# Kernel tuning notes

Measured on AMD Instinct MI355X. Metric: run time of the kernel, lower is better.

## Reference

```python
import jax, jax.numpy as jnp
import numpy as np

S, T = 8192, 16          # words per sentence, max chars per word
EC, HC = 64, 128         # char embed dim, char LSTM hidden
DW, HW = 300, 256        # word embed dim, word LSTM hidden
VW, VC, TAGS = 50000, 128, 50
DIN = DW + 2 * HC        # word LSTM input dim


def _lstm_scan(x, Wih, Whh, b, reverse=False):
    """Single-direction LSTM over x: [T, N, E] -> outputs [T, N, H].
    PyTorch gate order (i, f, g, o); b = b_ih + b_hh combined."""
    N = x.shape[1]
    H = Whh.shape[1]
    h0 = jnp.zeros((N, H), x.dtype)

    def cell(carry, xt):
        h, c = carry
        g = xt @ Wih.T + h @ Whh.T + b
        i, f, gg, o = jnp.split(g, 4, axis=-1)
        c = jax.nn.sigmoid(f) * c + jax.nn.sigmoid(i) * jnp.tanh(gg)
        h = jax.nn.sigmoid(o) * jnp.tanh(c)
        return (h, c), h

    _, hs = jax.lax.scan(cell, (h0, h0), x, reverse=reverse)
    return hs


def setup_inputs() -> dict:
    key = jax.random.key(0)
    ks = iter(jax.random.split(key, 40))
    p = lambda *shape: jax.random.normal(next(ks), shape, jnp.float32) * 0.05

    inp = {
        "word_ix": jax.random.randint(next(ks), (S,), 0, VW, jnp.int32),
        "char_ix": jax.random.randint(next(ks), (S, T), 0, VC, jnp.int32),
        "char_len": jax.random.randint(next(ks), (S,), 1, T + 1, jnp.int32),
        "word_emb": p(VW, DW),
        "char_emb": p(VC, EC),
        # char LSTM, 2 layers x 2 directions (dir axis leading)
        "cW_ih0": p(2, 4 * HC, EC), "cW_hh0": p(2, 4 * HC, HC), "cb0": p(2, 4 * HC),
        "cW_ih1": p(2, 4 * HC, 2 * HC), "cW_hh1": p(2, 4 * HC, HC), "cb1": p(2, 4 * HC),
        # word LSTM, 2 layers x 2 directions
        "wW_ih0": p(2, 4 * HW, DIN), "wW_hh0": p(2, 4 * HW, HW), "wb0": p(2, 4 * HW),
        "wW_ih1": p(2, 4 * HW, 2 * HW), "wW_hh1": p(2, 4 * HW, HW), "wb1": p(2, 4 * HW),
        "out_W": p(TAGS, 2 * HW), "out_b": p(TAGS),
    }
    return inp


def reference(word_ix, char_ix, char_len, word_emb, char_emb,
              cW_ih0, cW_hh0, cb0, cW_ih1, cW_hh1, cb1,
              wW_ih0, wW_hh0, wb0, wW_ih1, wW_hh1, wb1,
              out_W, out_b):
    # --- char LSTM: all words batched together ---
    x = char_emb[char_ix].transpose(1, 0, 2)  # [T, S, EC]
    # NOTE: original calls the bidirectional LSTM one char at a time while
    # carrying hidden state, so the "backward" direction also scans forward.
    h0f = _lstm_scan(x, cW_ih0[0], cW_hh0[0], cb0[0])
    h0b = _lstm_scan(x, cW_ih0[1], cW_hh0[1], cb0[1])
    o0 = jnp.concatenate([h0f, h0b], -1)       # [T, S, 2*HC]
    h1f = _lstm_scan(o0, cW_ih1[0], cW_hh1[0], cb1[0])
    h1b = _lstm_scan(o0, cW_ih1[1], cW_hh1[1], cb1[1])
    o1 = jnp.concatenate([h1f, h1b], -1)       # [T, S, 2*HC]
    # last valid char per word (ragged lengths)
    chars_repr = o1[char_len - 1, jnp.arange(S)]  # [S, 2*HC]

    # --- word LSTM: true biLSTM over the sentence, batch 1 ---
    wx = jnp.concatenate([word_emb[word_ix], chars_repr], -1)[:, None, :]  # [S,1,DIN]
    w0f = _lstm_scan(wx, wW_ih0[0], wW_hh0[0], wb0[0])
    w0b = _lstm_scan(wx, wW_ih0[1], wW_hh0[1], wb0[1], reverse=True)
    wo0 = jnp.concatenate([w0f, w0b], -1)      # [S, 1, 2*HW]
    w1f = _lstm_scan(wo0, wW_ih1[0], wW_hh1[0], wb1[0])
    w1b = _lstm_scan(wo0, wW_ih1[1], wW_hh1[1], wb1[1], reverse=True)
    wo1 = jnp.concatenate([w1f, w1b], -1).reshape(S, 2 * HW)

    logits = wo1 @ out_W.T + out_b             # [S, TAGS]
    return jax.nn.log_softmax(logits, axis=1)
```

## Files before the change

### kernel.cpp

```cpp
#include <hip/hip_runtime.h>
#include <math.h>


#define SW 8192
#define TC 16
#define ECD 64
#define HCD 128
#define DWD 300
#define HWD 256
#define DIND 556
#define NTAGS 50
#define SENT 0x40000000u

typedef float f32x4 __attribute__((ext_vector_type(4)));

__device__ __forceinline__ float sigf(float x) { return 1.f / (1.f + expf(-x)); }

#define BM 64
#define BN 64
#define BK 16

__global__ __launch_bounds__(256) void gemm2(
    const float* __restrict__ A1, int lda1, const int* __restrict__ idx1,
    const float* __restrict__ W1, int ldw1, int K1,
    const float* __restrict__ A2, int lda2,
    const float* __restrict__ W2, int ldw2, int K2,
    const float* __restrict__ bias, float* __restrict__ C, int N, int ldc)
{
    __shared__ float As[BK][BM + 4];
    __shared__ float Ws[BK][BN + 4];
    const int tid = threadIdx.x;
    const int m0 = blockIdx.y * BM;
    const int n0 = blockIdx.x * BN;
    const int tx = tid & 15, ty = tid >> 4;
    const int lr = tid >> 2;
    const int lk4 = (tid & 3) << 2;

    float acc[4][4] = {};

    for (int part = 0; part < 2; ++part) {
        const int K = part ? K2 : K1;
        if (K == 0) continue;
        const float* A = part ? A2 : A1;
        const float* W = part ? W2 : W1;
        const int* idx = part ? (const int*)nullptr : idx1;
        const int lda = part ? lda2 : lda1;
        const int ldw = part ? ldw2 : ldw1;
        const int arow = idx ? idx[m0 + lr] : (m0 + lr);
        const float* Ab = A + (size_t)arow * lda;
        const int wrow = n0 + lr;
        const bool wv = wrow < N;
        const float* Wb = W + (size_t)(wv ? wrow : 0) * ldw;
        for (int k0 = 0; k0 < K; k0 += BK) {
            const int k = k0 + lk4;
            float4 av, bv;
            if (k + 3 < K) {
                av = *(const float4*)(Ab + k);
            } else {
                av.x = (k + 0 < K) ? Ab[k + 0] : 0.f;
                av.y = (k + 1 < K) ? Ab[k + 1] : 0.f;
                av.z = (k + 2 < K) ? Ab[k + 2] : 0.f;
                av.w = (k + 3 < K) ? Ab[k + 3] : 0.f;
            }
            if (wv && (k + 3 < K)) {
                bv = *(const float4*)(Wb + k);
            } else if (wv) {
                bv.x = (k + 0 < K) ? Wb[k + 0] : 0.f;
                bv.y = (k + 1 < K) ? Wb[k + 1] : 0.f;
                bv.z = (k + 2 < K) ? Wb[k + 2] : 0.f;
                bv.w = (k + 3 < K) ? Wb[k + 3] : 0.f;
            } else {
                bv.x = bv.y = bv.z = bv.w = 0.f;
            }
            As[lk4 + 0][lr] = av.x;
            As[lk4 + 1][lr] = av.y;
            As[lk4 + 2][lr] = av.z;
            As[lk4 + 3][lr] = av.w;
            Ws[lk4 + 0][lr] = bv.x;
            Ws[lk4 + 1][lr] = bv.y;
            Ws[lk4 + 2][lr] = bv.z;
            Ws[lk4 + 3][lr] = bv.w;
            __syncthreads();
#pragma unroll
            for (int kk = 0; kk < BK; ++kk) {
                const float4 a = *(const float4*)&As[kk][ty << 2];
                const float4 b = *(const float4*)&Ws[kk][tx << 2];
                acc[0][0] += a.x * b.x; acc[0][1] += a.x * b.y; acc[0][2] += a.x * b.z; acc[0][3] += a.x * b.w;
                acc[1][0] += a.y * b.x; acc[1][1] += a.y * b.y; acc[1][2] += a.y * b.z; acc[1][3] += a.y * b.w;
                acc[2][0] += a.z * b.x; acc[2][1] += a.z * b.y; acc[2][2] += a.z * b.z; acc[2][3] += a.z * b.w;
                acc[3][0] += a.w * b.x; acc[3][1] += a.w * b.y; acc[3][2] += a.w * b.z; acc[3][3] += a.w * b.w;
            }
            __syncthreads();
        }
    }
#pragma unroll
    for (int i = 0; i < 4; ++i) {
        const int m = m0 + (ty << 2) + i;
#pragma unroll
        for (int j = 0; j < 4; ++j) {
            const int n = n0 + (tx << 2) + j;
            if (n < N) C[(size_t)m * ldc + n] = acc[i][j] + (bias ? bias[n] : 0.f);
        }
    }
}

__global__ __launch_bounds__(256) void build_cidx(const int* __restrict__ char_ix,
                                                  int* __restrict__ cidx)
{
    const int id = blockIdx.x * 256 + threadIdx.x;
    const int t = id >> 13, s = id & (SW - 1);
    cidx[id] = char_ix[s * TC + t];
}

__global__ __launch_bounds__(256) void lstm_cell_char(
    const float* __restrict__ gates, float* __restrict__ c, float* __restrict__ h,
    float* __restrict__ o_out, float* __restrict__ crepr,
    const int* __restrict__ char_len, int t)
{
    const int id = blockIdx.x * 256 + threadIdx.x;
    const int s = id >> 7, j = id & (HCD - 1);
    const float* g = gates + (size_t)s * 512;
    const float gi = g[j], gf = g[HCD + j], gg = g[2 * HCD + j], go = g[3 * HCD + j];
    const float cn = sigf(gf) * c[id] + sigf(gi) * tanhf(gg);
    const float hn = sigf(go) * tanhf(cn);
    c[id] = cn;
    h[id] = hn;
    if (o_out) o_out[(size_t)s * 256 + j] = hn;
    if (crepr && (char_len[s] - 1 == t)) crepr[(size_t)s * 256 + j] = hn;
}

__global__ __launch_bounds__(256) void fill_sentinel(float4* __restrict__ a, int n4)
{
    const int i = blockIdx.x * 256 + threadIdx.x;
    if (i < n4) a[i] = float4{2.f, 2.f, 2.f, 2.f};
}

__global__ __launch_bounds__(256, 1) void word_scan(
    const float* __restrict__ G,
    const float* __restrict__ Whh,
    float* __restrict__ out)
{
    const int d = blockIdx.x >> 4;
    const int bb = blockIdx.x & 15;
    const int tid = threadIdx.x;
    const int l = tid & 63;
    const int wave = tid >> 6;
    const int r = tid >> 2;
    const int cg = tid & 3;
    const int jj = r >> 2;
    const int g = r & 3;
    const int grow = (g << 8) + (bb << 4) + jj;

    __shared__ __align__(16) float hl[2][4 * 68];

    const float* wrow = Whh + ((size_t)d << 18) + (size_t)grow * 256 + (cg << 6);
    const float* Gd = G + ((size_t)d * SW * 1024);
    const int dcol = d << 8;
    const int tstart = d ? (SW - 1) : 0;
    const int tstep = d ? -1 : 1;
    float creg = 0.f;

    float gval = 0.f;
    if (cg == 0) gval = Gd[(size_t)tstart * 1024 + grow];

    for (int it = 0; it < SW; ++it) {
        const int t = tstart + tstep * it;
        float* hb = &hl[it & 1][0];

        f32x4 wv[16];
#pragma unroll
        for (int i = 0; i < 16; ++i) wv[i] = ((const f32x4*)wrow)[i];

        if (wave == 0) {
            f32x4 hv;
            if (it) {
                const int tp = t - tstep;
                const float* hp = out + (size_t)tp * 512 + dcol + (l << 2);
                for (;;) {
                    asm volatile("global_load_dwordx4 %0, %1, off sc0 sc1\n\t"
                                 "s_waitcnt vmcnt(0)"
                                 : "=v"(hv) : "v"(hp) : "memory");
                    const unsigned* u = (const unsigned*)&hv;
                    const bool bad = (u[0] == SENT) | (u[1] == SENT) |
                                     (u[2] == SENT) | (u[3] == SENT);
                    if (!__any(bad)) break;
                    __builtin_amdgcn_s_sleep(1);
                }
            } else {
                hv = f32x4{0.f, 0.f, 0.f, 0.f};
            }
            *(f32x4*)&hb[(l >> 4) * 68 + ((l & 15) << 2)] = hv;
        }
        __syncthreads();

        const f32x4* hp4 = (const f32x4*)&hb[cg * 68];
        float a0 = 0.f, a1 = 0.f, a2 = 0.f, a3 = 0.f;
#pragma unroll
        for (int i = 0; i < 16; ++i) {
            const f32x4 h4 = hp4[i];
            a0 = fmaf(wv[i][0], h4[0], a0);
            a1 = fmaf(wv[i][1], h4[1], a1);
            a2 = fmaf(wv[i][2], h4[2], a2);
            a3 = fmaf(wv[i][3], h4[3], a3);
        }
        float s = (a0 + a1) + (a2 + a3);
        s += __shfl_xor(s, 1);
        s += __shfl_xor(s, 2);
        s += gval;

        const float xx = (g == 2) ? (s + s) : s;
        const float sg = 1.f / (1.f + expf(-xx));
        const float act = (g == 2) ? (2.f * sg - 1.f) : sg;

        const int gb = l & 48;
        const float af = __shfl(act, gb + 4);
        const float ag = __shfl(act, gb + 8);
        const float ao = __shfl(act, gb + 12);
        if ((l & 15) == 0) {
            creg = af * creg + act * ag;
            const float hn = ao * tanhf(creg);
            const int j = (wave << 2) + (l >> 4);
            float* dst = out + (size_t)t * 512 + dcol + (bb << 4) + j;
            asm volatile("global_store_dword %0, %1, off sc0 sc1"
                         :: "v"(dst), "v"(hn) : "memory");
        }

        if (cg == 0 && it + 1 < SW)
            gval = Gd[(size_t)(t + tstep) * 1024 + grow];
    }
}

__global__ __launch_bounds__(256) void logsoftmax50(const float* __restrict__ X,
                                                    float* __restrict__ Y)
{
    const int gw = (blockIdx.x * 256 + threadIdx.x) >> 6;
    const int lane = threadIdx.x & 63;
    if (gw >= SW) return;
    const float v = (lane < NTAGS) ? X[(size_t)gw * NTAGS + lane] : -3.4e38f;
    float m = v;
#pragma unroll
    for (int o = 32; o; o >>= 1) m = fmaxf(m, __shfl_xor(m, o));
    const float e = (lane < NTAGS) ? expf(v - m) : 0.f;
    float sum = e;
#pragma unroll
    for (int o = 32; o; o >>= 1) sum += __shfl_xor(sum, o);
    if (lane < NTAGS) Y[(size_t)gw * NTAGS + lane] = v - m - logf(sum);
}

extern "C" void kernel_launch(void* const* d_in, const int* in_sizes, int n_in,
                              void* d_out, int out_size, void* d_ws, size_t ws_size,
                              hipStream_t stream)
{
    const int* word_ix  = (const int*)d_in[0];
    const int* char_ix  = (const int*)d_in[1];
    const int* char_len = (const int*)d_in[2];
    const float* word_emb = (const float*)d_in[3];
    const float* char_emb = (const float*)d_in[4];
    const float* cW_ih0 = (const float*)d_in[5];
    const float* cW_hh0 = (const float*)d_in[6];
    const float* cb0    = (const float*)d_in[7];
    const float* cW_ih1 = (const float*)d_in[8];
    const float* cW_hh1 = (const float*)d_in[9];
    const float* cb1    = (const float*)d_in[10];
    const float* wW_ih0 = (const float*)d_in[11];
    const float* wW_hh0 = (const float*)d_in[12];
    const float* wb0    = (const float*)d_in[13];
    const float* wW_ih1 = (const float*)d_in[14];
    const float* wW_hh1 = (const float*)d_in[15];
    const float* wb1    = (const float*)d_in[16];
    const float* out_W  = (const float*)d_in[17];
    const float* out_b  = (const float*)d_in[18];
    float* Y = (float*)d_out;
    (void)in_sizes; (void)n_in; (void)out_size; (void)ws_size;

    char* p = (char*)d_ws;
    auto alloc = [&](size_t bytes) { char* q = p; p += (bytes + 255) & ~(size_t)255; return q; };
    float* ch_h  = (float*)alloc(4ull * SW * HCD * 4);
    float* ch_c  = (float*)alloc(4ull * SW * HCD * 4);
    const size_t zbytes = (size_t)(p - (char*)d_ws);
    float* gates = (float*)alloc(2ull * SW * 512 * 4);
    float* o0s   = (float*)alloc((size_t)SW * 256 * 4);
    float* crepr = (float*)alloc((size_t)SW * 256 * 4);
    float* wG    = (float*)alloc(2ull * SW * 1024 * 4);
    float* wo0   = (float*)alloc((size_t)SW * 512 * 4);
    float* wo1   = (float*)alloc((size_t)SW * 512 * 4);
    int*   cidx  = (int*)  alloc((size_t)TC * SW * 4);

    hipMemsetAsync(d_ws, 0, zbytes, stream);
    fill_sentinel<<<(SW * 512 / 4 + 255) / 256, 256, 0, stream>>>((float4*)wo0, SW * 512 / 4);
    fill_sentinel<<<(SW * 512 / 4 + 255) / 256, 256, 0, stream>>>((float4*)wo1, SW * 512 / 4);
    build_cidx<<<TC * SW / 256, 256, 0, stream>>>(char_ix, cidx);

    for (int t = 0; t < TC; ++t) {
        for (int d = 0; d < 2; ++d)
            gemm2<<<dim3(512 / BN, SW / BM), 256, 0, stream>>>(
                char_emb, ECD, cidx + t * SW, cW_ih0 + (size_t)d * 512 * ECD, ECD, ECD,
                ch_h + (size_t)d * SW * HCD, HCD, cW_hh0 + (size_t)d * 512 * HCD, HCD, HCD,
                cb0 + d * 512, gates + (size_t)d * SW * 512, 512, 512);
        for (int d = 0; d < 2; ++d)
            lstm_cell_char<<<SW * HCD / 256, 256, 0, stream>>>(
                gates + (size_t)d * SW * 512, ch_c + (size_t)d * SW * HCD,
                ch_h + (size_t)d * SW * HCD, o0s + d * HCD, nullptr, nullptr, t);
        for (int d = 0; d < 2; ++d)
            gemm2<<<dim3(512 / BN, SW / BM), 256, 0, stream>>>(
                o0s, 256, nullptr, cW_ih1 + (size_t)d * 512 * 256, 256, 256,
                ch_h + (size_t)(2 + d) * SW * HCD, HCD, cW_hh1 + (size_t)d * 512 * HCD, HCD, HCD,
                cb1 + d * 512, gates + (size_t)d * SW * 512, 512, 512);
        for (int d = 0; d < 2; ++d)
            lstm_cell_char<<<SW * HCD / 256, 256, 0, stream>>>(
                gates + (size_t)d * SW * 512, ch_c + (size_t)(2 + d) * SW * HCD,
                ch_h + (size_t)(2 + d) * SW * HCD, nullptr, crepr + d * HCD, char_len, t);
    }

    for (int d = 0; d < 2; ++d)
        gemm2<<<dim3(1024 / BN, SW / BM), 256, 0, stream>>>(
            word_emb, DWD, word_ix, wW_ih0 + (size_t)d * 1024 * DIND, DIND, DWD,
            crepr, 256, wW_ih0 + (size_t)d * 1024 * DIND + DWD, DIND, 256,
            wb0 + d * 1024, wG + (size_t)d * SW * 1024, 1024, 1024);
    word_scan<<<32, 256, 0, stream>>>(wG, wW_hh0, wo0);

    for (int d = 0; d < 2; ++d)
        gemm2<<<dim3(1024 / BN, SW / BM), 256, 0, stream>>>(
            wo0, 512, nullptr, wW_ih1 + (size_t)d * 1024 * 512, 512, 512,
            nullptr, 0, nullptr, 0, 0,
            wb1 + d * 1024, wG + (size_t)d * SW * 1024, 1024, 1024);
    word_scan<<<32, 256, 0, stream>>>(wG, wW_hh1, wo1);

    gemm2<<<dim3(1, SW / BM), 256, 0, stream>>>(
        wo1, 512, nullptr, out_W, 512, 512,
        nullptr, 0, nullptr, 0, 0,
        out_b, gates, NTAGS, NTAGS);
    logsoftmax50<<<SW * 64 / 256, 256, 0, stream>>>(gates, Y);
}
```

Baseline: 30.40 ms.

## Pin word-scan blocks to one XCD, pack recurrent weights as bf16, relax polling

```diff
diff --git a/kernel.cpp b/kernel.cpp
--- a/kernel.cpp
+++ b/kernel.cpp
@@ -15,6 +15,12 @@
 typedef float f32x4 __attribute__((ext_vector_type(4)));
 
 __device__ __forceinline__ float sigf(float x) { return 1.f / (1.f + expf(-x)); }
+__device__ __forceinline__ float blo(unsigned u) { return __uint_as_float(u << 16); }
+__device__ __forceinline__ float bhi(unsigned u) { return __uint_as_float(u & 0xffff0000u); }
+__device__ __forceinline__ unsigned short f2bf(float x) {
+    unsigned u = __float_as_uint(x);
+    return (unsigned short)((u + 0x7fffu + ((u >> 16) & 1u)) >> 16);
+}
 
 #define BM 64
 #define BN 64
@@ -135,25 +141,53 @@
     if (i < n4) a[i] = float4{2.f, 2.f, 2.f, 2.f};
 }
 
+__global__ __launch_bounds__(256) void pack_whh(const float* __restrict__ Whh,
+                                                uint4* __restrict__ P)
+{
+    const int id = blockIdx.x * 256 + threadIdx.x;
+    const int tid = id & 255;
+    const int i = (id >> 8) & 7;
+    const int bb = (id >> 11) & 15;
+    const int d = (id >> 15) & 1;
+    const int j = tid >> 4, g = (tid >> 2) & 3, cg = tid & 3;
+    const int grow = (g << 8) + (bb << 4) + j;
+    const int col = (cg << 6) + (i << 3);
+    const float* src = Whh + ((size_t)d << 18) + (size_t)grow * 256 + col;
+    unsigned q[4];
+#pragma unroll
+    for (int m = 0; m < 4; ++m)
+        q[m] = (unsigned)f2bf(src[2 * m]) | ((unsigned)f2bf(src[2 * m + 1]) << 16);
+    P[id] = uint4{q[0], q[1], q[2], q[3]};
+}
+
 __global__ __launch_bounds__(256, 1) void word_scan(
     const float* __restrict__ G,
-    const float* __restrict__ Whh,
-    float* __restrict__ out)
-{
-    const int d = blockIdx.x >> 4;
-    const int bb = blockIdx.x & 15;
+    const uint4* __restrict__ Wp,
+    float* __restrict__ out,
+    int* __restrict__ ticket)
+{
+    unsigned xcd;
+    asm volatile("s_getreg_b32 %0, hwreg(HW_REG_XCC_ID)" : "=s"(xcd));
+    xcd &= 7;
+    __shared__ int rank_s;
+    if (threadIdx.x == 0) rank_s = atomicAdd(ticket + xcd, 1);
+    __syncthreads();
+    const int rank = rank_s;
+    if (rank >= 32) return;
+
+    const int d = rank >> 4;
+    const int bb = rank & 15;
     const int tid = threadIdx.x;
     const int l = tid & 63;
     const int wave = tid >> 6;
-    const int r = tid >> 2;
+    const int j = tid >> 4;
+    const int g = (tid >> 2) & 3;
     const int cg = tid & 3;
-    const int jj = r >> 2;
-    const int g = r & 3;
-    const int grow = (g << 8) + (bb << 4) + jj;
+    const int grow = (g << 8) + (bb << 4) + j;
 
     __shared__ __align__(16) float hl[2][4 * 68];
 
-    const float* wrow = Whh + ((size_t)d << 18) + (size_t)grow * 256 + (cg << 6);
+    const uint4* wp = Wp + (((size_t)(d * 16 + bb)) << 11) + tid;
     const float* Gd = G + ((size_t)d * SW * 1024);
     const int dcol = d << 8;
     const int tstart = d ? (SW - 1) : 0;
@@ -167,46 +201,60 @@
         const int t = tstart + tstep * it;
         float* hb = &hl[it & 1][0];
 
-        f32x4 wv[16];
-#pragma unroll
-        for (int i = 0; i < 16; ++i) wv[i] = ((const f32x4*)wrow)[i];
+        uint4 wch[8];
+#pragma unroll
+        for (int i = 0; i < 8; ++i) wch[i] = wp[i << 8];
 
         if (wave == 0) {
             f32x4 hv;
             if (it) {
                 const int tp = t - tstep;
                 const float* hp = out + (size_t)tp * 512 + dcol + (l << 2);
+                int tries = 0;
                 for (;;) {
-                    asm volatile("global_load_dwordx4 %0, %1, off sc0 sc1\n\t"
+                    asm volatile("global_load_dwordx4 %0, %1, off sc0\n\t"
                                  "s_waitcnt vmcnt(0)"
                                  : "=v"(hv) : "v"(hp) : "memory");
                     const unsigned* u = (const unsigned*)&hv;
-                    const bool bad = (u[0] == SENT) | (u[1] == SENT) |
-                                     (u[2] == SENT) | (u[3] == SENT);
+                    bool bad = (u[0] == SENT) | (u[1] == SENT) |
+                               (u[2] == SENT) | (u[3] == SENT);
                     if (!__any(bad)) break;
-                    __builtin_amdgcn_s_sleep(1);
+                    if ((++tries & 63) == 0) {
+                        asm volatile("global_load_dwordx4 %0, %1, off sc0 sc1\n\t"
+                                     "s_waitcnt vmcnt(0)"
+                                     : "=v"(hv) : "v"(hp) : "memory");
+                        bad = (u[0] == SENT) | (u[1] == SENT) |
+                              (u[2] == SENT) | (u[3] == SENT);
+                        if (!__any(bad)) break;
+                        __builtin_amdgcn_s_sleep(1);
+                    }
                 }
             } else {
                 hv = f32x4{0.f, 0.f, 0.f, 0.f};
             }
-            *(f32x4*)&hb[(l >> 4) * 68 + ((l & 15) << 2)] = hv;
+            *(f32x4*)&hb[(l >> 4) * 68 + ((l << 2) & 63)] = hv;
         }
         __syncthreads();
 
         const f32x4* hp4 = (const f32x4*)&hb[cg * 68];
-        float a0 = 0.f, a1 = 0.f, a2 = 0.f, a3 = 0.f;
-#pragma unroll
-        for (int i = 0; i < 16; ++i) {
-            const f32x4 h4 = hp4[i];
-            a0 = fmaf(wv[i][0], h4[0], a0);
-            a1 = fmaf(wv[i][1], h4[1], a1);
-            a2 = fmaf(wv[i][2], h4[2], a2);
-            a3 = fmaf(wv[i][3], h4[3], a3);
-        }
-        float s = (a0 + a1) + (a2 + a3);
-        s += __shfl_xor(s, 1);
-        s += __shfl_xor(s, 2);
-        s += gval;
+        float acc = 0.f;
+#pragma unroll
+        for (int i = 0; i < 8; ++i) {
+            const uint4 wv = wch[i];
+            const f32x4 h0 = hp4[2 * i];
+            const f32x4 h1 = hp4[2 * i + 1];
+            acc = fmaf(blo(wv.x), h0[0], acc);
+            acc = fmaf(bhi(wv.x), h0[1], acc);
+            acc = fmaf(blo(wv.y), h0[2], acc);
+            acc = fmaf(bhi(wv.y), h0[3], acc);
+            acc = fmaf(blo(wv.z), h1[0], acc);
+            acc = fmaf(bhi(wv.z), h1[1], acc);
+            acc = fmaf(blo(wv.w), h1[2], acc);
+            acc = fmaf(bhi(wv.w), h1[3], acc);
+        }
+        acc += __shfl_xor(acc, 1);
+        acc += __shfl_xor(acc, 2);
+        const float s = acc + gval;
 
         const float xx = (g == 2) ? (s + s) : s;
         const float sg = 1.f / (1.f + expf(-xx));
@@ -219,8 +267,9 @@
         if ((l & 15) == 0) {
             creg = af * creg + act * ag;
             const float hn = ao * tanhf(creg);
-            const int j = (wave << 2) + (l >> 4);
             float* dst = out + (size_t)t * 512 + dcol + (bb << 4) + j;
+            asm volatile("global_store_dword %0, %1, off"
+                         :: "v"(dst), "v"(hn) : "memory");
             asm volatile("global_store_dword %0, %1, off sc0 sc1"
                          :: "v"(dst), "v"(hn) : "memory");
         }
@@ -275,6 +324,7 @@
 
     char* p = (char*)d_ws;
     auto alloc = [&](size_t bytes) { char* q = p; p += (bytes + 255) & ~(size_t)255; return q; };
+    int*   ticket = (int*) alloc(2ull * 8 * 4);
     float* ch_h  = (float*)alloc(4ull * SW * HCD * 4);
     float* ch_c  = (float*)alloc(4ull * SW * HCD * 4);
     const size_t zbytes = (size_t)(p - (char*)d_ws);
@@ -284,11 +334,15 @@
     float* wG    = (float*)alloc(2ull * SW * 1024 * 4);
     float* wo0   = (float*)alloc((size_t)SW * 512 * 4);
     float* wo1   = (float*)alloc((size_t)SW * 512 * 4);
+    uint4* Wp0   = (uint4*)alloc(65536ull * 16);
+    uint4* Wp1   = (uint4*)alloc(65536ull * 16);
     int*   cidx  = (int*)  alloc((size_t)TC * SW * 4);
 
     hipMemsetAsync(d_ws, 0, zbytes, stream);
     fill_sentinel<<<(SW * 512 / 4 + 255) / 256, 256, 0, stream>>>((float4*)wo0, SW * 512 / 4);
     fill_sentinel<<<(SW * 512 / 4 + 255) / 256, 256, 0, stream>>>((float4*)wo1, SW * 512 / 4);
+    pack_whh<<<256, 256, 0, stream>>>(wW_hh0, Wp0);
+    pack_whh<<<256, 256, 0, stream>>>(wW_hh1, Wp1);
     build_cidx<<<TC * SW / 256, 256, 0, stream>>>(char_ix, cidx);
 
     for (int t = 0; t < TC; ++t) {
@@ -317,14 +371,14 @@
             word_emb, DWD, word_ix, wW_ih0 + (size_t)d * 1024 * DIND, DIND, DWD,
             crepr, 256, wW_ih0 + (size_t)d * 1024 * DIND + DWD, DIND, 256,
             wb0 + d * 1024, wG + (size_t)d * SW * 1024, 1024, 1024);
-    word_scan<<<32, 256, 0, stream>>>(wG, wW_hh0, wo0);
+    word_scan<<<256, 256, 0, stream>>>(wG, Wp0, wo0, ticket);
 
     for (int d = 0; d < 2; ++d)
         gemm2<<<dim3(1024 / BN, SW / BM), 256, 0, stream>>>(
             wo0, 512, nullptr, wW_ih1 + (size_t)d * 1024 * 512, 512, 512,
             nullptr, 0, nullptr, 0, 0,
             wb1 + d * 1024, wG + (size_t)d * SW * 1024, 1024, 1024);
-    word_scan<<<32, 256, 0, stream>>>(wG, wW_hh1, wo1);
+    word_scan<<<256, 256, 0, stream>>>(wG, Wp1, wo1, ticket + 8);
 
     gemm2<<<dim3(1, SW / BM), 256, 0, stream>>>(
         wo1, 512, nullptr, out_W, 512, 512,
```

Measured after the change: 106.9 ms. 3.52x slower.
